# Kernel optimization log

Measured on AMD Instinct MI355X. Metric: run time of the kernel, lower is better.

Reference implementation:

```python
import jax, jax.numpy as jnp
import numpy as np

D_MODEL = 192
D_INNER = 384          # expand * d_model
D_STATE = 64
NHEADS = 8             # d_inner / headdim
HEADDIM = 48
D_CONV = 4
CONV_DIM = D_INNER + 2 * D_STATE   # 512 (ngroups=1)
D_IN_PROJ = 2 * D_INNER + 2 * D_STATE + NHEADS  # 904
MIX = 32
EPS = 1e-5


def silu(v):
    return v * jax.nn.sigmoid(v)


def setup_inputs() -> dict:
    key = jax.random.key(0)
    ks = jax.random.split(key, 16)
    B, L, C = 4, 4096, 4
    x = jax.random.normal(ks[0], (B, L, C), jnp.float32)
    Wfc = jax.random.normal(ks[1], (C, D_MODEL), jnp.float32) * 0.3
    bfc = jnp.zeros((D_MODEL,), jnp.float32)
    W_in = jax.random.normal(ks[2], (D_MODEL, D_IN_PROJ), jnp.float32) * 0.02
    conv_w = jax.random.normal(ks[3], (D_CONV, 1, CONV_DIM), jnp.float32) * 0.2  # depthwise (W,I/g,O)
    conv_b = jnp.zeros((CONV_DIM,), jnp.float32)
    # dt_bias = inv_softplus(dt_init) with dt_init ~ U(1e-3, 0.1)
    dt_init = jax.random.uniform(ks[4], (NHEADS,), jnp.float32, 1e-3, 0.1)
    dt_bias = jnp.log(jnp.expm1(dt_init))
    A_log = jnp.log(jax.random.uniform(ks[5], (NHEADS,), jnp.float32, 1.0, 16.0))
    Dparam = jnp.ones((NHEADS,), jnp.float32)
    norm_w = jnp.ones((D_INNER,), jnp.float32)
    W_out = jax.random.normal(ks[6], (D_INNER, D_MODEL), jnp.float32) * 0.02
    W1 = jax.random.normal(ks[7], (D_MODEL, MIX), jnp.float32) * 0.05
    b1 = jnp.zeros((MIX,), jnp.float32)
    W2 = jax.random.normal(ks[8], (MIX, MIX), jnp.float32) * 0.1
    b2 = jnp.zeros((MIX,), jnp.float32)
    Wo = jax.random.normal(ks[9], (MIX, 1), jnp.float32) * 0.1
    bo = jnp.zeros((1,), jnp.float32)
    return {"x": x, "Wfc": Wfc, "bfc": bfc, "W_in": W_in, "conv_w": conv_w,
            "conv_b": conv_b, "dt_bias": dt_bias, "A_log": A_log, "Dparam": Dparam,
            "norm_w": norm_w, "W_out": W_out, "W1": W1, "b1": b1, "W2": W2,
            "b2": b2, "Wo": Wo, "bo": bo}


def _mamba2(h, W_in, conv_w, conv_b, dt_bias, A_log, Dparam, norm_w, W_out):
    B, L, _ = h.shape
    zxbcdt = h @ W_in                                    # (B,L,904)
    z = zxbcdt[..., :D_INNER]
    xBC = zxbcdt[..., D_INNER:D_INNER + CONV_DIM]
    dt = jax.nn.softplus(zxbcdt[..., -NHEADS:] + dt_bias)  # (B,L,H)
    # causal depthwise conv1d
    xBC = jnp.pad(xBC, ((0, 0), (D_CONV - 1, 0), (0, 0)))
    xBC = jax.lax.conv_general_dilated(
        xBC, conv_w, window_strides=(1,), padding="VALID",
        dimension_numbers=("NWC", "WIO", "NWC"), feature_group_count=CONV_DIM)
    xBC = silu(xBC + conv_b)                             # (B,L,512)
    xs = xBC[..., :D_INNER].reshape(B, L, NHEADS, HEADDIM)
    Bm = xBC[..., D_INNER:D_INNER + D_STATE]             # (B,L,N)
    Cm = xBC[..., D_INNER + D_STATE:]                    # (B,L,N)
    A = -jnp.exp(A_log)                                  # (H,)
    dA = jnp.exp(dt * A)                                 # (B,L,H)

    def step(hstate, inp):
        dA_t, dt_t, B_t, x_t, C_t = inp                  # (B,H),(B,H),(B,N),(B,H,P),(B,N)
        dBx_t = jnp.einsum("bh,bn,bhp->bhpn", dt_t, B_t, x_t)
        hstate = dA_t[:, :, None, None] * hstate + dBx_t  # (B,H,P,N)
        y_t = jnp.einsum("bhpn,bn->bhp", hstate, C_t)
        return hstate, y_t

    h0 = jnp.zeros((B, NHEADS, HEADDIM, D_STATE), h.dtype)
    xs_t = jnp.swapaxes(xs, 0, 1)
    _, ys = jax.lax.scan(step, h0, (jnp.swapaxes(dA, 0, 1), jnp.swapaxes(dt, 0, 1),
                                    jnp.swapaxes(Bm, 0, 1), xs_t, jnp.swapaxes(Cm, 0, 1)))
    y = jnp.swapaxes(ys, 0, 1) + Dparam[None, None, :, None] * xs  # (B,L,H,P)
    y = y.reshape(B, L, D_INNER)
    # gated RMSNorm: rmsnorm(y * silu(z)) * weight
    y = y * silu(z)
    y = y * jax.lax.rsqrt(jnp.mean(y * y, axis=-1, keepdims=True) + EPS) * norm_w
    return y @ W_out                                     # (B,L,d_model)


def reference(x, Wfc, bfc, W_in, conv_w, conv_b, dt_bias, A_log, Dparam,
              norm_w, W_out, W1, b1, W2, b2, Wo, bo):
    h = x @ Wfc + bfc                                    # input_fc
    h = _mamba2(h, W_in, conv_w, conv_b, dt_bias, A_log, Dparam, norm_w, W_out)
    m = jax.nn.relu(h @ W1 + b1)
    m = jax.nn.relu(m @ W2 + b2)                         # dropout = identity (eval)
    m = jnp.mean(m, axis=1)                              # pool over time
    angle = (m @ Wo + bo)[:, 0]
    return angle
```

## Files before the change

kernel.cpp:

```cpp
#include <hip/hip_runtime.h>
#include <math.h>


#define BDIM 4
#define LDIM 4096
#define BL (BDIM*LDIM)
#define QC 64
#define NC (LDIM/QC)
#define BH (BDIM*NH)
#define NH 8

#define OFF_W    0u
#define OFF_Z    3145728u
#define OFF_T    9437184u
#define OFF_XS   17825792u
#define OFF_BM   24117248u
#define OFF_CM   25165824u
#define OFF_DT   26214400u
#define OFF_LAC  26345472u
#define OFF_SP   26476544u
#define OFF_Y    32768000u
#define OFF_MACC 39059456u

typedef unsigned short ushort_t;
typedef __attribute__((ext_vector_type(8))) short bf16x8;
typedef __attribute__((ext_vector_type(4))) float f32x4;

__device__ __forceinline__ float sigmoidf_(float x){ return 1.0f/(1.0f+__expf(-x)); }
__device__ __forceinline__ ushort_t f2bf(float x){
  unsigned int u = __float_as_uint(x);
  u += 0x7fffu + ((u>>16)&1u);
  return (ushort_t)(u>>16);
}
__device__ __forceinline__ float bf2f(ushort_t h){
  return __uint_as_float(((unsigned int)h)<<16);
}

__global__ void k_prep(const float* __restrict__ Wfc, const float* __restrict__ bfc,
                       const float* __restrict__ W_in, const float* __restrict__ W_out,
                       const float* __restrict__ W1,
                       float* __restrict__ Weff, float* __restrict__ beff,
                       float* __restrict__ Weff2, float* __restrict__ macc){
  int blk = blockIdx.x, tid = threadIdx.x;
  if (blk < 4){
    int n = blk*256 + tid;
    if (n >= 904) return;
    float a0=0.f,a1=0.f,a2=0.f,a3=0.f,ab=0.f;
    for (int d=0; d<192; d++){
      float w = W_in[(size_t)d*904 + n];
      a0 = fmaf(Wfc[d], w, a0);
      a1 = fmaf(Wfc[192+d], w, a1);
      a2 = fmaf(Wfc[384+d], w, a2);
      a3 = fmaf(Wfc[576+d], w, a3);
      ab = fmaf(bfc[d], w, ab);
    }
    Weff[n] = a0; Weff[904+n] = a1; Weff[1808+n] = a2; Weff[2712+n] = a3;
    beff[n] = ab;
  } else {
    if (blk == 4 && tid < 128) macc[tid] = 0.f;
    int g = (blk-4)*256 + tid;
    int i = g>>5, j = g&31;
    float a = 0.f;
    for (int d=0; d<192; d++) a = fmaf(W_out[(size_t)i*192+d], W1[d*32+j], a);
    Weff2[g] = a;
  }
}

__global__ __launch_bounds__(256) void k_ipc(
    const float* __restrict__ x, const float* __restrict__ Weff,
    const float* __restrict__ beff, const float* __restrict__ conv_w,
    const float* __restrict__ conv_b, const float* __restrict__ dt_bias,
    ushort_t* __restrict__ xs_h, ushort_t* __restrict__ xs_l,
    ushort_t* __restrict__ Bm_h, ushort_t* __restrict__ Bm_l,
    ushort_t* __restrict__ Cm_h, ushort_t* __restrict__ Cm_l,
    float* __restrict__ dtb){
  __shared__ float sx[4][4];
  int bl = blockIdx.x, tid = threadIdx.x;
  int l = bl & 4095, b = bl >> 12;
  if (tid < 16){
    int k = tid>>2, r = tid&3;
    int ll = l-3+k;
    sx[k][r] = (ll>=0) ? x[(size_t)(b*4096+ll)*4 + r] : 0.f;
  }
  __syncthreads();
  if (tid < 8){
    float raw = beff[896+tid];
    #pragma unroll
    for (int r=0;r<4;r++) raw = fmaf(sx[3][r], Weff[r*904+896+tid], raw);
    float xx = raw + dt_bias[tid];
    float dtv = (xx > 20.f) ? xx : log1pf(__expf(xx));
    dtb[(size_t)(b*8+tid)*4096 + l] = dtv;
  }
  #pragma unroll
  for (int half=0; half<2; half++){
    int c = tid + half*256;
    float w0 = Weff[384+c];
    float w1 = Weff[904+384+c];
    float w2 = Weff[1808+384+c];
    float w3 = Weff[2712+384+c];
    float bb = beff[384+c];
    float acc = conv_b[c];
    #pragma unroll
    for (int k=0;k<4;k++){
      int ll = l-3+k;
      float xv = bb;
      xv = fmaf(sx[k][0], w0, xv);
      xv = fmaf(sx[k][1], w1, xv);
      xv = fmaf(sx[k][2], w2, xv);
      xv = fmaf(sx[k][3], w3, xv);
      if (ll < 0) xv = 0.f;
      acc = fmaf(conv_w[k*512+c], xv, acc);
    }
    float v = acc * sigmoidf_(acc);
    ushort_t hi = f2bf(v);
    ushort_t lo = f2bf(v - bf2f(hi));
    if (c < 384){
      int hh = c / 48, p = c - hh*48;
      size_t idx = (size_t)((b*8+hh)*4096 + l)*48 + p;
      xs_h[idx] = hi; xs_l[idx] = lo;
    } else if (c < 448){
      size_t idx = (size_t)bl*64 + (c-384);
      Bm_h[idx] = hi; Bm_l[idx] = lo;
    } else {
      size_t idx = (size_t)bl*64 + (c-448);
      Cm_h[idx] = hi; Cm_l[idx] = lo;
    }
  }
}

__global__ __launch_bounds__(256, 3) void k_phase1(
    const float* __restrict__ dtbuf,
    const ushort_t* __restrict__ Bm_h, const ushort_t* __restrict__ Bm_l,
    const ushort_t* __restrict__ xs_h, const ushort_t* __restrict__ xs_l,
    const float* __restrict__ A_log,
    float* __restrict__ T, float* __restrict__ lac){
  __shared__ __align__(16) ushort_t sBh[64*72], sBl[64*72];
  __shared__ __align__(16) ushort_t sXh[48*72], sXl[48*72];
  __shared__ float sdt[64], sla[64], sw[64];
  int tid = threadIdx.x, blk = blockIdx.x;
  int bh = blk >> 6, k = blk & 63;
  int b = bh >> 3, hh = bh & 7;
  int t0 = k*64;
  int w = tid>>6, lane = tid&63, l15 = lane&15, quad = lane>>4;

  if (tid < 64) sdt[tid] = dtbuf[(size_t)bh*4096 + t0 + tid];
  __syncthreads();
  if (tid == 0){
    float eA = __expf(A_log[hh]);
    float cum = 0.f;
    for (int i=0;i<64;i++){ cum -= sdt[i]*eA; sla[i] = cum; }
  }
  __syncthreads();
  if (tid < 64){
    sw[tid] = __expf(sla[63]-sla[tid])*sdt[tid];
    lac[(size_t)blk*64 + tid] = sla[tid];
  }
  __syncthreads();
  {
    int s2 = (tid&31)*2, ng = (tid>>5)*8;
    size_t base0 = (size_t)(b*4096+t0+s2)*64 + ng;
    ushort_t h0a[8], l0a[8], h1a[8], l1a[8];
    *(uint4*)h0a = *(const uint4*)(Bm_h + base0);
    *(uint4*)l0a = *(const uint4*)(Bm_l + base0);
    *(uint4*)h1a = *(const uint4*)(Bm_h + base0 + 64);
    *(uint4*)l1a = *(const uint4*)(Bm_l + base0 + 64);
    float w0 = sw[s2], w1 = sw[s2+1];
    #pragma unroll
    for (int c=0;c<8;c++){
      float f0 = (bf2f(h0a[c]) + bf2f(l0a[c])) * w0;
      float f1 = (bf2f(h1a[c]) + bf2f(l1a[c])) * w1;
      ushort_t h0 = f2bf(f0), h1 = f2bf(f1);
      ushort_t lo0 = f2bf(f0-bf2f(h0)), lo1 = f2bf(f1-bf2f(h1));
      int o = (ng+c)*72 + s2;
      *(unsigned int*)&sBh[o] = (unsigned int)h0 | ((unsigned int)h1<<16);
      *(unsigned int*)&sBl[o] = (unsigned int)lo0 | ((unsigned int)lo1<<16);
    }
  }
  {
    int s2 = (tid>>3)*2, p0 = (tid&7)*6;
    const ushort_t* xh0 = xs_h + (size_t)(bh*4096+t0+s2)*48 + p0;
    const ushort_t* xl0 = xs_l + (size_t)(bh*4096+t0+s2)*48 + p0;
    #pragma unroll
    for (int c=0;c<6;c++){
      unsigned int hv = (unsigned int)xh0[c] | ((unsigned int)xh0[48+c]<<16);
      unsigned int lv = (unsigned int)xl0[c] | ((unsigned int)xl0[48+c]<<16);
      int o = (p0+c)*72 + s2;
      *(unsigned int*)&sXh[o] = hv;
      *(unsigned int*)&sXl[o] = lv;
    }
  }
  __syncthreads();
  f32x4 acc[3];
  #pragma unroll
  for (int t=0;t<3;t++) acc[t] = (f32x4)(0.f);
  #pragma unroll
  for (int ks=0;ks<2;ks++){
    int bo = (w*16+l15)*72 + ks*32 + quad*8;
    bf16x8 bbh = *(bf16x8*)&sBh[bo];
    bf16x8 bbl = *(bf16x8*)&sBl[bo];
    #pragma unroll
    for (int pt=0;pt<3;pt++){
      int xo = (pt*16+l15)*72 + ks*32 + quad*8;
      bf16x8 xah = *(bf16x8*)&sXh[xo];
      bf16x8 xal = *(bf16x8*)&sXl[xo];
      acc[pt] = __builtin_amdgcn_mfma_f32_16x16x32_bf16(xah, bbh, acc[pt], 0,0,0);
      acc[pt] = __builtin_amdgcn_mfma_f32_16x16x32_bf16(xah, bbl, acc[pt], 0,0,0);
      acc[pt] = __builtin_amdgcn_mfma_f32_16x16x32_bf16(xal, bbh, acc[pt], 0,0,0);
    }
  }
  {
    float* dst = T + (size_t)blk*3072;
    #pragma unroll
    for (int pt=0;pt<3;pt++)
      #pragma unroll
      for (int r=0;r<4;r++)
        dst[(pt*16+quad*4+r)*64 + w*16 + l15] = acc[pt][r];
  }
}

__global__ __launch_bounds__(256) void k_phase2p(
    const float* __restrict__ T, const float* __restrict__ lac, float* __restrict__ Sp){
  __shared__ __align__(16) float sT[64*64];
  __shared__ __align__(16) float sW[64][68];
  __shared__ float sc[64];
  int tid = threadIdx.x;
  int bh = blockIdx.x, es = blockIdx.y;
  #pragma unroll
  for (int r=0;r<4;r++){
    int idx = tid + r*256;
    int row = idx>>4, c4 = (idx&15)*4;
    *(float4*)&sT[row*64 + c4] = *(const float4*)(T + (size_t)(bh*64+row)*3072 + es*64 + c4);
  }
  if (tid < 64) sc[tid] = __expf(lac[(size_t)(bh*64+tid)*64 + 63]);
  __syncthreads();
  if (tid < 64){
    int k = tid;
    float w = 1.f;
    for (int j=63; j>=0; --j){
      bool a = (j < k);
      sW[j][k] = a ? w : 0.f;
      if (a) w *= sc[j];
    }
  }
  __syncthreads();
  int k0 = (tid>>4)*4, e0 = (tid&15)*4;
  float acc[4][4];
  #pragma unroll
  for (int i=0;i<4;i++)
    #pragma unroll
    for (int j=0;j<4;j++) acc[i][j]=0.f;
  int jmax = k0+2; if (jmax > 62) jmax = 62;
  for (int j=0; j<=jmax; ++j){
    float wv[4], tv[4];
    *(float4*)wv = *(float4*)&sW[j][k0];
    *(float4*)tv = *(float4*)&sT[j*64 + e0];
    #pragma unroll
    for (int i=0;i<4;i++)
      #pragma unroll
      for (int e=0;e<4;e++) acc[i][e] = fmaf(wv[i], tv[e], acc[i][e]);
  }
  #pragma unroll
  for (int i=0;i<4;i++){
    float4 o; o.x=acc[i][0]; o.y=acc[i][1]; o.z=acc[i][2]; o.w=acc[i][3];
    *(float4*)(Sp + (size_t)(bh*64+k0+i)*3072 + es*64 + e0) = o;
  }
}

__global__ __launch_bounds__(256, 3) void k_phase3(
    const float* __restrict__ dtbuf, const float* __restrict__ lac,
    const ushort_t* __restrict__ Bm_h, const ushort_t* __restrict__ Bm_l,
    const ushort_t* __restrict__ Cm_h, const ushort_t* __restrict__ Cm_l,
    const ushort_t* __restrict__ xs_h, const ushort_t* __restrict__ xs_l,
    const float* __restrict__ Sp, const float* __restrict__ Dparam,
    ushort_t* __restrict__ y16){
  __shared__ __align__(16) ushort_t sCh[64*72], sCl[64*72];
  __shared__ __align__(16) ushort_t sBh[64*72], sBl[64*72];
  __shared__ __align__(16) ushort_t sXh[48*72], sXl[48*72];
  __shared__ float sla[64], sdt[64];
  int tid = threadIdx.x, blk = blockIdx.x;
  int bh = blk>>6, k = blk&63, b = bh>>3, hh = bh&7, t0 = k*64;
  int w = tid>>6, lane = tid&63, l15 = lane&15, quad = lane>>4;

  if (tid < 64){
    sdt[tid] = dtbuf[(size_t)bh*4096 + t0 + tid];
    sla[tid] = lac[(size_t)blk*64 + tid];
  }
  {
    int row = tid>>2, ng = (tid&3)*16;
    size_t gb = (size_t)(b*4096+t0+row)*64 + ng;
    int o = row*72 + ng;
    *(uint4*)&sCh[o]   = *(const uint4*)(Cm_h + gb);
    *(uint4*)&sCh[o+8] = *(const uint4*)(Cm_h + gb + 8);
    *(uint4*)&sCl[o]   = *(const uint4*)(Cm_l + gb);
    *(uint4*)&sCl[o+8] = *(const uint4*)(Cm_l + gb + 8);
    *(uint4*)&sBh[o]   = *(const uint4*)(Bm_h + gb);
    *(uint4*)&sBh[o+8] = *(const uint4*)(Bm_h + gb + 8);
    *(uint4*)&sBl[o]   = *(const uint4*)(Bm_l + gb);
    *(uint4*)&sBl[o+8] = *(const uint4*)(Bm_l + gb + 8);
  }
  {
    int s2 = (tid>>3)*2, p0 = (tid&7)*6;
    const ushort_t* xh0 = xs_h + (size_t)(bh*4096+t0+s2)*48 + p0;
    const ushort_t* xl0 = xs_l + (size_t)(bh*4096+t0+s2)*48 + p0;
    #pragma unroll
    for (int c=0;c<6;c++){
      unsigned int hv = (unsigned int)xh0[c] | ((unsigned int)xh0[48+c]<<16);
      unsigned int lv = (unsigned int)xl0[c] | ((unsigned int)xl0[48+c]<<16);
      int o = (p0+c)*72 + s2;
      *(unsigned int*)&sXh[o] = hv;
      *(unsigned int*)&sXl[o] = lv;
    }
  }
  __syncthreads();

  f32x4 gacc[4];
  #pragma unroll
  for (int t=0;t<4;t++) gacc[t] = (f32x4)(0.f);
  {
    bf16x8 cah[2], cal[2];
    #pragma unroll
    for (int ks=0;ks<2;ks++){
      int ao = (w*16+l15)*72 + ks*32 + quad*8;
      cah[ks] = *(bf16x8*)&sCh[ao];
      cal[ks] = *(bf16x8*)&sCl[ao];
    }
    for (int bs=0; bs<=w; ++bs){
      #pragma unroll
      for (int ks=0;ks<2;ks++){
        int bo = (bs*16+l15)*72 + ks*32 + quad*8;
        bf16x8 bhf = *(bf16x8*)&sBh[bo];
        bf16x8 blf = *(bf16x8*)&sBl[bo];
        gacc[bs] = __builtin_amdgcn_mfma_f32_16x16x32_bf16(cah[ks], bhf, gacc[bs], 0,0,0);
        gacc[bs] = __builtin_amdgcn_mfma_f32_16x16x32_bf16(cah[ks], blf, gacc[bs], 0,0,0);
        gacc[bs] = __builtin_amdgcn_mfma_f32_16x16x32_bf16(cal[ks], bhf, gacc[bs], 0,0,0);
      }
    }
  }
  __syncthreads();

  for (int bs=0; bs<=w; ++bs){
    #pragma unroll
    for (int r=0;r<4;r++){
      int i = w*16 + quad*4 + r;
      int s = bs*16 + l15;
      float v = 0.f;
      if (s <= i) v = gacc[bs][r] * __expf(sla[i]-sla[s]) * sdt[s];
      ushort_t hi = f2bf(v);
      sBh[i*72+s] = hi;
      sBl[i*72+s] = f2bf(v - bf2f(hi));
    }
  }
  if (w==0){
    #pragma unroll
    for (int r=0;r<4;r++){ sBh[(quad*4+r)*72 + 16+l15] = 0; sBl[(quad*4+r)*72 + 16+l15] = 0; }
  }
  if (w==2){
    #pragma unroll
    for (int r=0;r<4;r++){ sBh[(32+quad*4+r)*72 + 48+l15] = 0; sBl[(32+quad*4+r)*72 + 48+l15] = 0; }
  }
  __syncthreads();

  float4 spv[3][2][2];
  {
    const float* sp0 = Sp + (size_t)blk*3072;
    #pragma unroll
    for (int pt=0;pt<3;pt++)
      #pragma unroll
      for (int ks=0;ks<2;ks++){
        const float* p = sp0 + (pt*16+l15)*64 + ks*32 + quad*8;
        spv[pt][ks][0] = *(const float4*)(p);
        spv[pt][ks][1] = *(const float4*)(p+4);
      }
  }

  f32x4 accI[3], accA[3];
  #pragma unroll
  for (int t=0;t<3;t++){ accI[t] = (f32x4)(0.f); accA[t] = (f32x4)(0.f); }
  int nks = (w>=2) ? 2 : 1;
  for (int ks=0; ks<nks; ++ks){
    int go = (w*16+l15)*72 + ks*32 + quad*8;
    bf16x8 gbh = *(bf16x8*)&sBh[go];
    bf16x8 gbl = *(bf16x8*)&sBl[go];
    #pragma unroll
    for (int pt=0;pt<3;pt++){
      int xo = (pt*16+l15)*72 + ks*32 + quad*8;
      bf16x8 xah = *(bf16x8*)&sXh[xo];
      bf16x8 xal = *(bf16x8*)&sXl[xo];
      accI[pt] = __builtin_amdgcn_mfma_f32_16x16x32_bf16(xah, gbh, accI[pt], 0,0,0);
      accI[pt] = __builtin_amdgcn_mfma_f32_16x16x32_bf16(xah, gbl, accI[pt], 0,0,0);
      accI[pt] = __builtin_amdgcn_mfma_f32_16x16x32_bf16(xal, gbh, accI[pt], 0,0,0);
    }
  }
  #pragma unroll
  for (int ks=0; ks<2; ++ks){
    int co = (w*16+l15)*72 + ks*32 + quad*8;
    bf16x8 cbh = *(bf16x8*)&sCh[co];
    bf16x8 cbl = *(bf16x8*)&sCl[co];
    #pragma unroll
    for (int pt=0;pt<3;pt++){
      const float* vv = (const float*)&spv[pt][ks][0];
      bf16x8 pah, pal;
      #pragma unroll
      for (int c=0;c<8;c++){
        ushort_t hi = f2bf(vv[c]);
        pah[c] = (short)hi;
        pal[c] = (short)f2bf(vv[c] - bf2f(hi));
      }
      accA[pt] = __builtin_amdgcn_mfma_f32_16x16x32_bf16(pah, cbh, accA[pt], 0,0,0);
      accA[pt] = __builtin_amdgcn_mfma_f32_16x16x32_bf16(pah, cbl, accA[pt], 0,0,0);
      accA[pt] = __builtin_amdgcn_mfma_f32_16x16x32_bf16(pal, cbh, accA[pt], 0,0,0);
    }
  }
  {
    int i = w*16 + l15;
    float eli = __expf(sla[i]);
    float Dh = Dparam[hh];
    ushort_t* ybase = y16 + (size_t)(b*4096+t0+i)*384 + hh*48;
    #pragma unroll
    for (int pt=0;pt<3;pt++)
      #pragma unroll
      for (int r=0;r<4;r++){
        int p = pt*16 + quad*4 + r;
        float xf = bf2f(sXh[p*72 + i]) + bf2f(sXl[p*72 + i]);
        ybase[p] = f2bf(accI[pt][r] + eli*accA[pt][r] + Dh*xf);
      }
  }
}

__global__ __launch_bounds__(256) void k_gate(
    const float* __restrict__ x, const float* __restrict__ Weff,
    const float* __restrict__ beff, const float* __restrict__ norm_w,
    const ushort_t* __restrict__ y16, ushort_t* __restrict__ yn16){
  int tid = threadIdx.x;
  int w = tid>>6, lane = tid&63;
  int e0 = lane*6;
  float W0[6],W1v[6],W2v[6],W3v[6],bv[6],nw[6];
  #pragma unroll
  for (int c=0;c<6;c++){
    int e = e0+c;
    W0[c]=Weff[e]; W1v[c]=Weff[904+e]; W2v[c]=Weff[1808+e]; W3v[c]=Weff[2712+e];
    bv[c]=beff[e]; nw[c]=norm_w[e];
  }
  #pragma unroll
  for (int t=0;t<4;t++){
    int bl = blockIdx.x*16 + w*4 + t;
    float4 xv = *(const float4*)(x + (size_t)bl*4);
    float g[6]; float ss = 0.f;
    #pragma unroll
    for (int c=0;c<6;c++){
      float zv = bv[c];
      zv = fmaf(xv.x, W0[c], zv);
      zv = fmaf(xv.y, W1v[c], zv);
      zv = fmaf(xv.z, W2v[c], zv);
      zv = fmaf(xv.w, W3v[c], zv);
      float yv = bf2f(y16[(size_t)bl*384 + e0 + c]);
      float gg = yv * (zv * sigmoidf_(zv));
      g[c] = gg; ss += gg*gg;
    }
    #pragma unroll
    for (int off=32; off>0; off>>=1) ss += __shfl_xor(ss, off);
    float rms = rsqrtf(ss*(1.f/384.f) + 1e-5f);
    #pragma unroll
    for (int c=0;c<6;c++)
      yn16[(size_t)bl*384 + e0 + c] = f2bf(g[c]*rms*nw[c]);
  }
}

__global__ __launch_bounds__(256) void k_mlp2(
    const ushort_t* __restrict__ yn16, const float* __restrict__ Weff2,
    const float* __restrict__ b1, const float* __restrict__ W2,
    const float* __restrict__ b2, float* __restrict__ macc){
  __shared__ __align__(16) float sW[384][32];
  __shared__ __align__(16) float sm1[64][33];
  __shared__ __align__(16) float sW2[32][32];
  __shared__ __align__(16) float sm2[64][33];
  int tid = threadIdx.x;
  int tok0 = blockIdx.x*64;
  int b = tok0 >> 12;
  #pragma unroll
  for (int r=0;r<12;r++){
    int idx = tid + r*256;
    int row = idx>>3, c4 = (idx&7)*4;
    *(float4*)&sW[row][c4] = *(const float4*)(Weff2 + (size_t)idx*4);
  }
  {
    int row = tid>>3, c4 = (tid&7)*4;
    *(float4*)&sW2[row][c4] = *(const float4*)(W2 + row*32 + c4);
  }
  __syncthreads();
  {
    int tk = tid>>3, j0 = (tid&7)*4;
    float a0[4], a1[4];
    #pragma unroll
    for (int j=0;j<4;j++){ a0[j] = b1[j0+j]; a1[j] = a0[j]; }
    const ushort_t* y0 = yn16 + (size_t)(tok0+tk)*384;
    const ushort_t* y1 = yn16 + (size_t)(tok0+tk+32)*384;
    for (int k8=0;k8<48;k8++){
      ushort_t ua[8], ub[8];
      *(uint4*)ua = *(const uint4*)(y0 + k8*8);
      *(uint4*)ub = *(const uint4*)(y1 + k8*8);
      #pragma unroll
      for (int c=0;c<8;c++){
        float va = bf2f(ua[c]), vb = bf2f(ub[c]);
        float w[4]; *(float4*)w = *(float4*)&sW[k8*8+c][j0];
        #pragma unroll
        for (int j=0;j<4;j++){ a0[j] = fmaf(va, w[j], a0[j]); a1[j] = fmaf(vb, w[j], a1[j]); }
      }
    }
    #pragma unroll
    for (int j=0;j<4;j++){
      sm1[tk][j0+j]    = fmaxf(a0[j], 0.f);
      sm1[tk+32][j0+j] = fmaxf(a1[j], 0.f);
    }
  }
  __syncthreads();
  {
    int tk = tid>>3, j0 = (tid&7)*4;
    float a0[4], a1[4];
    #pragma unroll
    for (int j=0;j<4;j++){ a0[j] = b2[j0+j]; a1[j] = a0[j]; }
    #pragma unroll
    for (int kk=0;kk<32;kk++){
      float va = sm1[tk][kk];
      float vb = sm1[tk+32][kk];
      float w[4]; *(float4*)w = *(float4*)&sW2[kk][j0];
      #pragma unroll
      for (int j=0;j<4;j++){ a0[j] = fmaf(va, w[j], a0[j]); a1[j] = fmaf(vb, w[j], a1[j]); }
    }
    #pragma unroll
    for (int j=0;j<4;j++){
      sm2[tk][j0+j]    = fmaxf(a0[j], 0.f);
      sm2[tk+32][j0+j] = fmaxf(a1[j], 0.f);
    }
  }
  __syncthreads();
  if (tid < 32){
    float t = 0.f;
    #pragma unroll
    for (int tok=0;tok<64;tok++) t += sm2[tok][tid];
    atomicAdd(&macc[b*32 + tid], t);
  }
}

__global__ void k_final(const float* __restrict__ macc, const float* __restrict__ Wo,
                        const float* __restrict__ bo, float* __restrict__ out){
  int tid = threadIdx.x;
  if (tid < 4){
    float acc = bo[0];
    #pragma unroll
    for (int j=0;j<32;j++) acc = fmaf(macc[tid*32+j]*(1.f/4096.f), Wo[j], acc);
    out[tid] = acc;
  }
}

extern "C" void kernel_launch(void* const* d_in, const int* in_sizes, int n_in,
                              void* d_out, int out_size, void* d_ws, size_t ws_size,
                              hipStream_t stream){
  const float* x      = (const float*)d_in[0];
  const float* Wfc    = (const float*)d_in[1];
  const float* bfc    = (const float*)d_in[2];
  const float* W_in   = (const float*)d_in[3];
  const float* conv_w = (const float*)d_in[4];
  const float* conv_b = (const float*)d_in[5];
  const float* dt_bias= (const float*)d_in[6];
  const float* A_log  = (const float*)d_in[7];
  const float* Dparam = (const float*)d_in[8];
  const float* norm_w = (const float*)d_in[9];
  const float* W_out  = (const float*)d_in[10];
  const float* W1     = (const float*)d_in[11];
  const float* b1     = (const float*)d_in[12];
  const float* W2     = (const float*)d_in[13];
  const float* b2     = (const float*)d_in[14];
  const float* Wo     = (const float*)d_in[15];
  const float* bo     = (const float*)d_in[16];
  float* ws  = (float*)d_ws;
  float* out = (float*)d_out;

  float* Weff  = ws + OFF_W;
  float* beff  = ws + OFF_W + 4096;
  float* Weff2 = ws + OFF_W + 8192;
  ushort_t* yn16 = (ushort_t*)(ws + OFF_Z);
  float* Tb    = ws + OFF_T;
  ushort_t* xs_h = (ushort_t*)(ws + OFF_XS);
  ushort_t* xs_l = xs_h + 6291456u;
  ushort_t* Bm_h = (ushort_t*)(ws + OFF_BM);
  ushort_t* Bm_l = Bm_h + 1048576u;
  ushort_t* Cm_h = (ushort_t*)(ws + OFF_CM);
  ushort_t* Cm_l = Cm_h + 1048576u;
  float* dtb   = ws + OFF_DT;
  float* lacb  = ws + OFF_LAC;
  float* Spb   = ws + OFF_SP;
  ushort_t* y16 = (ushort_t*)(ws + OFF_Y);
  float* macc  = ws + OFF_MACC;

  k_prep<<<dim3(52), dim3(256), 0, stream>>>(Wfc, bfc, W_in, W_out, W1,
                                             Weff, beff, Weff2, macc);
  k_ipc<<<dim3(BL), dim3(256), 0, stream>>>(x, Weff, beff, conv_w, conv_b,
                                            dt_bias, xs_h, xs_l, Bm_h, Bm_l,
                                            Cm_h, Cm_l, dtb);
  k_phase1<<<dim3(BH*NC), dim3(256), 0, stream>>>(dtb, Bm_h, Bm_l, xs_h, xs_l,
                                                  A_log, Tb, lacb);
  k_phase2p<<<dim3(BH,48), dim3(256), 0, stream>>>(Tb, lacb, Spb);
  k_phase3<<<dim3(BH*NC), dim3(256), 0, stream>>>(dtb, lacb, Bm_h, Bm_l,
                                                  Cm_h, Cm_l, xs_h, xs_l,
                                                  Spb, Dparam, y16);
  k_gate<<<dim3(BL/16), dim3(256), 0, stream>>>(x, Weff, beff, norm_w, y16, yn16);
  k_mlp2<<<dim3(BL/64), dim3(256), 0, stream>>>(yn16, Weff2, b1, W2, b2, macc);
  k_final<<<dim3(1), dim3(64), 0, stream>>>(macc, Wo, bo, out);
}
```

Baseline: 209.4 us.

## Store chunk states as split bf16, load C/B fragments directly, fold norm weight

```diff
diff --git a/kernel.cpp b/kernel.cpp
--- a/kernel.cpp
+++ b/kernel.cpp
@@ -38,7 +38,7 @@
 
 __global__ void k_prep(const float* __restrict__ Wfc, const float* __restrict__ bfc,
                        const float* __restrict__ W_in, const float* __restrict__ W_out,
-                       const float* __restrict__ W1,
+                       const float* __restrict__ W1, const float* __restrict__ norm_w,
                        float* __restrict__ Weff, float* __restrict__ beff,
                        float* __restrict__ Weff2, float* __restrict__ macc){
   int blk = blockIdx.x, tid = threadIdx.x;
@@ -62,7 +62,7 @@
     int i = g>>5, j = g&31;
     float a = 0.f;
     for (int d=0; d<192; d++) a = fmaf(W_out[(size_t)i*192+d], W1[d*32+j], a);
-    Weff2[g] = a;
+    Weff2[g] = a * norm_w[i];
   }
 }
 
@@ -219,7 +219,8 @@
 }
 
 __global__ __launch_bounds__(256) void k_phase2p(
-    const float* __restrict__ T, const float* __restrict__ lac, float* __restrict__ Sp){
+    const float* __restrict__ T, const float* __restrict__ lac,
+    ushort_t* __restrict__ Sp_h, ushort_t* __restrict__ Sp_l){
   __shared__ __align__(16) float sT[64*64];
   __shared__ __align__(16) float sW[64][68];
   __shared__ float sc[64];
@@ -261,8 +262,18 @@
   }
   #pragma unroll
   for (int i=0;i<4;i++){
-    float4 o; o.x=acc[i][0]; o.y=acc[i][1]; o.z=acc[i][2]; o.w=acc[i][3];
-    *(float4*)(Sp + (size_t)(bh*64+k0+i)*3072 + es*64 + e0) = o;
+    ushort4 h4, l4;
+    ushort_t* hp = (ushort_t*)&h4;
+    ushort_t* lp = (ushort_t*)&l4;
+    #pragma unroll
+    for (int e=0;e<4;e++){
+      ushort_t hi = f2bf(acc[i][e]);
+      hp[e] = hi;
+      lp[e] = f2bf(acc[i][e] - bf2f(hi));
+    }
+    size_t o = (size_t)(bh*64+k0+i)*3072 + es*64 + e0;
+    *(ushort4*)(Sp_h + o) = h4;
+    *(ushort4*)(Sp_l + o) = l4;
   }
 }
 
@@ -271,9 +282,8 @@
     const ushort_t* __restrict__ Bm_h, const ushort_t* __restrict__ Bm_l,
     const ushort_t* __restrict__ Cm_h, const ushort_t* __restrict__ Cm_l,
     const ushort_t* __restrict__ xs_h, const ushort_t* __restrict__ xs_l,
-    const float* __restrict__ Sp, const float* __restrict__ Dparam,
-    ushort_t* __restrict__ y16){
-  __shared__ __align__(16) ushort_t sCh[64*72], sCl[64*72];
+    const ushort_t* __restrict__ Sp_h, const ushort_t* __restrict__ Sp_l,
+    const float* __restrict__ Dparam, ushort_t* __restrict__ y16){
   __shared__ __align__(16) ushort_t sBh[64*72], sBl[64*72];
   __shared__ __align__(16) ushort_t sXh[48*72], sXl[48*72];
   __shared__ float sla[64], sdt[64];
@@ -286,19 +296,6 @@
     sla[tid] = lac[(size_t)blk*64 + tid];
   }
   {
-    int row = tid>>2, ng = (tid&3)*16;
-    size_t gb = (size_t)(b*4096+t0+row)*64 + ng;
-    int o = row*72 + ng;
-    *(uint4*)&sCh[o]   = *(const uint4*)(Cm_h + gb);
-    *(uint4*)&sCh[o+8] = *(const uint4*)(Cm_h + gb + 8);
-    *(uint4*)&sCl[o]   = *(const uint4*)(Cm_l + gb);
-    *(uint4*)&sCl[o+8] = *(const uint4*)(Cm_l + gb + 8);
-    *(uint4*)&sBh[o]   = *(const uint4*)(Bm_h + gb);
-    *(uint4*)&sBh[o+8] = *(const uint4*)(Bm_h + gb + 8);
-    *(uint4*)&sBl[o]   = *(const uint4*)(Bm_l + gb);
-    *(uint4*)&sBl[o+8] = *(const uint4*)(Bm_l + gb + 8);
-  }
-  {
     int s2 = (tid>>3)*2, p0 = (tid&7)*6;
     const ushort_t* xh0 = xs_h + (size_t)(bh*4096+t0+s2)*48 + p0;
     const ushort_t* xl0 = xs_l + (size_t)(bh*4096+t0+s2)*48 + p0;
@@ -311,29 +308,28 @@
       *(unsigned int*)&sXl[o] = lv;
     }
   }
-  __syncthreads();
-
+  bf16x8 cah[2], cal[2];
+  {
+    const ushort_t* ch = Cm_h + (size_t)(b*4096+t0+w*16+l15)*64;
+    const ushort_t* cl = Cm_l + (size_t)(b*4096+t0+w*16+l15)*64;
+    #pragma unroll
+    for (int ks=0;ks<2;ks++){
+      cah[ks] = *(const bf16x8*)(ch + ks*32 + quad*8);
+      cal[ks] = *(const bf16x8*)(cl + ks*32 + quad*8);
+    }
+  }
   f32x4 gacc[4];
   #pragma unroll
   for (int t=0;t<4;t++) gacc[t] = (f32x4)(0.f);
-  {
-    bf16x8 cah[2], cal[2];
+  for (int bs=0; bs<=w; ++bs){
+    size_t brow = (size_t)(b*4096+t0+bs*16+l15)*64;
     #pragma unroll
     for (int ks=0;ks<2;ks++){
-      int ao = (w*16+l15)*72 + ks*32 + quad*8;
-      cah[ks] = *(bf16x8*)&sCh[ao];
-      cal[ks] = *(bf16x8*)&sCl[ao];
-    }
-    for (int bs=0; bs<=w; ++bs){
-      #pragma unroll
-      for (int ks=0;ks<2;ks++){
-        int bo = (bs*16+l15)*72 + ks*32 + quad*8;
-        bf16x8 bhf = *(bf16x8*)&sBh[bo];
-        bf16x8 blf = *(bf16x8*)&sBl[bo];
-        gacc[bs] = __builtin_amdgcn_mfma_f32_16x16x32_bf16(cah[ks], bhf, gacc[bs], 0,0,0);
-        gacc[bs] = __builtin_amdgcn_mfma_f32_16x16x32_bf16(cah[ks], blf, gacc[bs], 0,0,0);
-        gacc[bs] = __builtin_amdgcn_mfma_f32_16x16x32_bf16(cal[ks], bhf, gacc[bs], 0,0,0);
-      }
+      bf16x8 bhf = *(const bf16x8*)(Bm_h + brow + ks*32 + quad*8);
+      bf16x8 blf = *(const bf16x8*)(Bm_l + brow + ks*32 + quad*8);
+      gacc[bs] = __builtin_amdgcn_mfma_f32_16x16x32_bf16(cah[ks], bhf, gacc[bs], 0,0,0);
+      gacc[bs] = __builtin_amdgcn_mfma_f32_16x16x32_bf16(cah[ks], blf, gacc[bs], 0,0,0);
+      gacc[bs] = __builtin_amdgcn_mfma_f32_16x16x32_bf16(cal[ks], bhf, gacc[bs], 0,0,0);
     }
   }
   __syncthreads();
@@ -358,18 +354,18 @@
     #pragma unroll
     for (int r=0;r<4;r++){ sBh[(32+quad*4+r)*72 + 48+l15] = 0; sBl[(32+quad*4+r)*72 + 48+l15] = 0; }
   }
-  __syncthreads();
-
-  float4 spv[3][2][2];
-  {
-    const float* sp0 = Sp + (size_t)blk*3072;
+
+  bf16x8 pah[3][2], pal[3][2];
+  {
+    const ushort_t* sph = Sp_h + (size_t)blk*3072;
+    const ushort_t* spl = Sp_l + (size_t)blk*3072;
     #pragma unroll
     for (int pt=0;pt<3;pt++)
       #pragma unroll
       for (int ks=0;ks<2;ks++){
-        const float* p = sp0 + (pt*16+l15)*64 + ks*32 + quad*8;
-        spv[pt][ks][0] = *(const float4*)(p);
-        spv[pt][ks][1] = *(const float4*)(p+4);
+        size_t o = (size_t)(pt*16+l15)*64 + ks*32 + quad*8;
+        pah[pt][ks] = *(const bf16x8*)(sph + o);
+        pal[pt][ks] = *(const bf16x8*)(spl + o);
       }
   }
 
@@ -393,22 +389,11 @@
   }
   #pragma unroll
   for (int ks=0; ks<2; ++ks){
-    int co = (w*16+l15)*72 + ks*32 + quad*8;
-    bf16x8 cbh = *(bf16x8*)&sCh[co];
-    bf16x8 cbl = *(bf16x8*)&sCl[co];
     #pragma unroll
     for (int pt=0;pt<3;pt++){
-      const float* vv = (const float*)&spv[pt][ks][0];
-      bf16x8 pah, pal;
-      #pragma unroll
-      for (int c=0;c<8;c++){
-        ushort_t hi = f2bf(vv[c]);
-        pah[c] = (short)hi;
-        pal[c] = (short)f2bf(vv[c] - bf2f(hi));
-      }
-      accA[pt] = __builtin_amdgcn_mfma_f32_16x16x32_bf16(pah, cbh, accA[pt], 0,0,0);
-      accA[pt] = __builtin_amdgcn_mfma_f32_16x16x32_bf16(pah, cbl, accA[pt], 0,0,0);
-      accA[pt] = __builtin_amdgcn_mfma_f32_16x16x32_bf16(pal, cbh, accA[pt], 0,0,0);
+      accA[pt] = __builtin_amdgcn_mfma_f32_16x16x32_bf16(pah[pt][ks], cah[ks], accA[pt], 0,0,0);
+      accA[pt] = __builtin_amdgcn_mfma_f32_16x16x32_bf16(pah[pt][ks], cal[ks], accA[pt], 0,0,0);
+      accA[pt] = __builtin_amdgcn_mfma_f32_16x16x32_bf16(pal[pt][ks], cah[ks], accA[pt], 0,0,0);
     }
   }
   {
@@ -429,17 +414,17 @@
 
 __global__ __launch_bounds__(256) void k_gate(
     const float* __restrict__ x, const float* __restrict__ Weff,
-    const float* __restrict__ beff, const float* __restrict__ norm_w,
+    const float* __restrict__ beff,
     const ushort_t* __restrict__ y16, ushort_t* __restrict__ yn16){
   int tid = threadIdx.x;
   int w = tid>>6, lane = tid&63;
   int e0 = lane*6;
-  float W0[6],W1v[6],W2v[6],W3v[6],bv[6],nw[6];
+  float W0[6],W1v[6],W2v[6],W3v[6],bv[6];
   #pragma unroll
   for (int c=0;c<6;c++){
     int e = e0+c;
     W0[c]=Weff[e]; W1v[c]=Weff[904+e]; W2v[c]=Weff[1808+e]; W3v[c]=Weff[2712+e];
-    bv[c]=beff[e]; nw[c]=norm_w[e];
+    bv[c]=beff[e];
   }
   #pragma unroll
   for (int t=0;t<4;t++){
@@ -462,7 +447,7 @@
     float rms = rsqrtf(ss*(1.f/384.f) + 1e-5f);
     #pragma unroll
     for (int c=0;c<6;c++)
-      yn16[(size_t)bl*384 + e0 + c] = f2bf(g[c]*rms*nw[c]);
+      yn16[(size_t)bl*384 + e0 + c] = f2bf(g[c]*rms);
   }
 }
 
@@ -589,22 +574,23 @@
   ushort_t* Cm_l = Cm_h + 1048576u;
   float* dtb   = ws + OFF_DT;
   float* lacb  = ws + OFF_LAC;
-  float* Spb   = ws + OFF_SP;
+  ushort_t* Sp_h = (ushort_t*)(ws + OFF_SP);
+  ushort_t* Sp_l = Sp_h + 6291456u;
   ushort_t* y16 = (ushort_t*)(ws + OFF_Y);
   float* macc  = ws + OFF_MACC;
 
-  k_prep<<<dim3(52), dim3(256), 0, stream>>>(Wfc, bfc, W_in, W_out, W1,
+  k_prep<<<dim3(52), dim3(256), 0, stream>>>(Wfc, bfc, W_in, W_out, W1, norm_w,
                                              Weff, beff, Weff2, macc);
   k_ipc<<<dim3(BL), dim3(256), 0, stream>>>(x, Weff, beff, conv_w, conv_b,
                                             dt_bias, xs_h, xs_l, Bm_h, Bm_l,
                                             Cm_h, Cm_l, dtb);
   k_phase1<<<dim3(BH*NC), dim3(256), 0, stream>>>(dtb, Bm_h, Bm_l, xs_h, xs_l,
                                                   A_log, Tb, lacb);
-  k_phase2p<<<dim3(BH,48), dim3(256), 0, stream>>>(Tb, lacb, Spb);
+  k_phase2p<<<dim3(BH,48), dim3(256), 0, stream>>>(Tb, lacb, Sp_h, Sp_l);
   k_phase3<<<dim3(BH*NC), dim3(256), 0, stream>>>(dtb, lacb, Bm_h, Bm_l,
                                                   Cm_h, Cm_l, xs_h, xs_l,
-                                                  Spb, Dparam, y16);
-  k_gate<<<dim3(BL/16), dim3(256), 0, stream>>>(x, Weff, beff, norm_w, y16, yn16);
+                                                  Sp_h, Sp_l, Dparam, y16);
+  k_gate<<<dim3(BL/16), dim3(256), 0, stream>>>(x, Weff, beff, y16, yn16);
   k_mlp2<<<dim3(BL/64), dim3(256), 0, stream>>>(yn16, Weff2, b1, W2, b2, macc);
   k_final<<<dim3(1), dim3(64), 0, stream>>>(macc, Wo, bo, out);
 }
```

Result: slower. 216.1 us (+3.2%).
